# Kernel tuning notes

Measured on AMD Instinct MI355X. Metric: run time of the kernel, lower is better.

Reference implementation:

```python
import jax, jax.numpy as jnp
import numpy as np

BS = 8192
NUM_CLASSES = 400
D = 768


def _bilin_from_14(m14, Y, X, eH, eW):
    # Value of bilinear-resize(m14 -> (eH,eW)) at integer pixel (Y,X), computed on the fly.
    # torch F.interpolate(align_corners=False): src = (dst+0.5)*in/out - 0.5, clamped at 0.
    # m14: (bs,14,14); Y,X: (bs,14) float integer-valued coords; eH,eW: (bs,) float.
    sy = jnp.maximum((Y + 0.5) * 14.0 / eH[:, None] - 0.5, 0.0)
    sx = jnp.maximum((X + 0.5) * 14.0 / eW[:, None] - 0.5, 0.0)
    r0f = jnp.floor(sy); c0f = jnp.floor(sx)
    r0 = r0f.astype(jnp.int32); r1 = jnp.minimum(r0 + 1, 13)
    c0 = c0f.astype(jnp.int32); c1 = jnp.minimum(c0 + 1, 13)
    fy = sy - r0f; fx = sx - c0f
    b = jnp.arange(m14.shape[0])[:, None, None]
    g00 = m14[b, r0[:, :, None], c0[:, None, :]]
    g01 = m14[b, r0[:, :, None], c1[:, None, :]]
    g10 = m14[b, r1[:, :, None], c0[:, None, :]]
    g11 = m14[b, r1[:, :, None], c1[:, None, :]]
    wy = fy[:, :, None]; wx = fx[:, None, :]
    return g00 * (1 - wy) * (1 - wx) + g01 * (1 - wy) * wx + g10 * wy * (1 - wx) + g11 * wy * wx


def _get_mask(attn, o_pos, e_pos):
    # Fused, fully-batched equivalent of the per-sample python loop:
    #   resize 14x14 -> (eH,eW) bilinear; crop (top,left,oH,oW); resize -> 14x14 bilinear.
    # The final resize only reads the intermediate grid at 4 integer points per output
    # pixel, so we evaluate those points lazily via _bilin_from_14 (exact, no Emax grid).
    bs = attn.shape[0]
    m14 = attn.reshape(bs, 14, 14)
    eH = e_pos[:, 2].astype(jnp.float32); eW = e_pos[:, 3].astype(jnp.float32)
    top = (o_pos[:, 0] - e_pos[:, 0]).astype(jnp.float32)
    left = (o_pos[:, 1] - e_pos[:, 1]).astype(jnp.float32)
    oH = o_pos[:, 2].astype(jnp.float32); oW = o_pos[:, 3].astype(jnp.float32)
    i = jnp.arange(14, dtype=jnp.float32)[None, :]
    ty = jnp.maximum((i + 0.5) * oH[:, None] / 14.0 - 0.5, 0.0)  # (bs,14) coords in crop
    tx = jnp.maximum((i + 0.5) * oW[:, None] / 14.0 - 0.5, 0.0)
    y0 = jnp.floor(ty); y1 = jnp.minimum(y0 + 1.0, oH[:, None] - 1.0); wy = ty - y0
    x0 = jnp.floor(tx); x1 = jnp.minimum(x0 + 1.0, oW[:, None] - 1.0); wx = tx - x0
    Y0 = top[:, None] + y0; Y1 = top[:, None] + y1  # absolute rows in (eH,eW) grid
    X0 = left[:, None] + x0; X1 = left[:, None] + x1
    v00 = _bilin_from_14(m14, Y0, X0, eH, eW)
    v01 = _bilin_from_14(m14, Y0, X1, eH, eW)
    v10 = _bilin_from_14(m14, Y1, X0, eH, eW)
    v11 = _bilin_from_14(m14, Y1, X1, eH, eW)
    wyc = wy[:, :, None]; wxc = wx[:, None, :]
    out = v00 * (1 - wyc) * (1 - wxc) + v01 * (1 - wyc) * wxc + v10 * wyc * (1 - wxc) + v11 * wyc * wxc
    return out.reshape(bs, 196)


def _get_att_mask(attention, ratio=0.5):
    bs = attention.shape[0]
    a14 = attention.reshape(bs, 14, 14)
    # bilinear 14->7 with align_corners=False samples at frac 0.5 == 2x2 average pool
    a7 = a14.reshape(bs, 7, 2, 7, 2).mean(axis=(2, 4))
    flat = a7.reshape(bs, 49)
    n_keep = int(49 * ratio) + 1  # argsort desc, take top N+1 = 25
    _, idx = jax.lax.top_k(flat, n_keep)
    masks = jnp.ones((bs, 49), dtype=bool)
    masks = masks.at[jnp.arange(bs)[:, None], idx].set(False)
    m7 = masks.reshape(bs, 7, 7)
    full = jnp.repeat(jnp.repeat(m7, 2, axis=1), 2, axis=2)
    return full.reshape(bs, 196)


def setup_inputs() -> dict:
    key = jax.random.key(0)
    k1, k2, k3 = jax.random.split(key, 3)
    attn = jax.random.uniform(k1, (BS, 196), dtype=jnp.float32)
    rng = np.random.default_rng(0)
    IMG = 224
    eH = rng.integers(112, IMG + 1, BS); eW = rng.integers(112, IMG + 1, BS)
    eT = rng.integers(0, IMG - eH + 1); eL = rng.integers(0, IMG - eW + 1)
    def box():
        h = rng.integers(56, eH + 1); w = rng.integers(56, eW + 1)
        t = eT + rng.integers(0, eH - h + 1); l = eL + rng.integers(0, eW - w + 1)
        return np.stack([t, l, h, w], axis=1)
    e = np.stack([eT, eL, eH, eW], axis=1)
    pos = np.stack([box(), box(), e], axis=1).astype(np.int32)  # (BS,3,4)
    image_embed = jax.random.normal(k2, (2 * BS, D), dtype=jnp.float32)
    W = jax.random.normal(k3, (NUM_CLASSES, D), dtype=jnp.float32) * 0.02
    b = jnp.zeros((NUM_CLASSES,), dtype=jnp.float32)
    return {"attn": attn, "pos": jnp.asarray(pos), "image_embed": image_embed, "W": W, "b": b}


def reference(attn, pos, image_embed, W, b):
    cm1 = _get_mask(attn, pos[:, 0], pos[:, 2])
    mask1 = _get_att_mask(cm1)
    cm2 = _get_mask(attn, pos[:, 1], pos[:, 2])
    mask2 = _get_att_mask(cm2)
    mask = jnp.concatenate([mask1, mask2], axis=0)  # (2*bs,196) bool, fed to masked encoder
    logits = image_embed @ W.T + b
    return logits, mask
```

## Files before the change

kernel.cpp:

```cpp
#include <hip/hip_runtime.h>
#include <hip/hip_bf16.h>
#include <stdint.h>
#include <type_traits>

#define BSAMP 8192
#define NCLS 400
#define DIM 768
#define LOGITS_SIZE (16384LL * 400LL)
#define GEMM_BLOCKS 1280
#define MASK_BLOCKS 4096
#define W_ELEMS (NCLS * DIM)

typedef __attribute__((ext_vector_type(8))) short short8;
typedef __attribute__((ext_vector_type(4))) float floatx4;

__device__ inline unsigned int packbf(float a, float b) {
    unsigned int ua = __float_as_uint(a) + 0x8000u;
    unsigned int ub = __float_as_uint(b) + 0x8000u;
    return __builtin_amdgcn_perm(ub, ua, 0x07060302u);
}

__device__ inline short8 cvt8(float4 lo, float4 hi) {
    union { unsigned int u[4]; short8 s; } r;
    r.u[0] = packbf(lo.x, lo.y);
    r.u[1] = packbf(lo.z, lo.w);
    r.u[2] = packbf(hi.x, hi.y);
    r.u[3] = packbf(hi.z, hi.w);
    return r.s;
}

__device__ inline void gload16(const void* g, void* l) {
    __builtin_amdgcn_global_load_lds((const __attribute__((address_space(1))) void*)g,
                                     (__attribute__((address_space(3))) void*)l, 16, 0, 0);
}

__global__ void cvtW_kernel(const float* __restrict__ W, unsigned short* __restrict__ ws) {
    int i = (blockIdx.x * 256 + threadIdx.x) * 4;
    if (i < W_ELEMS) {
        float4 f = *(const float4*)(W + i);
        uint2 r;
        r.x = packbf(f.x, f.y);
        r.y = packbf(f.z, f.w);
        *(uint2*)(ws + i) = r;
    }
}

__device__ inline float tap4(const float* m14, int r0, int c0, float fy, float fx) {
    int r1 = min(r0 + 1, 13);
    int c1 = min(c0 + 1, 13);
    float g00 = m14[r0 * 14 + c0];
    float g01 = m14[r0 * 14 + c1];
    float g10 = m14[r1 * 14 + c0];
    float g11 = m14[r1 * 14 + c1];
    return g00 * (1.f - fy) * (1.f - fx) + g01 * (1.f - fy) * fx +
           g10 * fy * (1.f - fx) + g11 * fy * fx;
}

struct GemmSm { unsigned short B[2][4][80 * 32]; };

template <bool USE_WS>
__global__ __launch_bounds__(256, 4) void gemm_kernel(const float* __restrict__ E,
                                                      const float* __restrict__ W,
                                                      const float* __restrict__ bias,
                                                      const unsigned short* __restrict__ wsW,
                                                      float* __restrict__ out) {
    __shared__ __align__(16) GemmSm sg;

    const int bx = blockIdx.x;
    const int t  = threadIdx.x;
    const int wv = t >> 6, ln = t & 63;

    const int xcd = bx & 7;
    const int j   = bx >> 3;
    const int n0  = (j % 5) * 80;
    const int m0  = (xcd * 32 + j / 5) * 64;
    const int quad = ln >> 4, l16 = ln & 15;

    const float* aptr = E + (size_t)(m0 + wv * 16 + l16) * DIM + quad * 8;

    floatx4 acc[5];
#pragma unroll
    for (int ni = 0; ni < 5; ++ni) acc[ni] = (floatx4){0.f, 0.f, 0.f, 0.f};

    if constexpr (USE_WS) {
        auto stageB = [&](int s, int buf) {
            unsigned short* dst = &sg.B[buf][wv][0];
            const int rr = ln >> 2, ch = ln & 3;
#pragma unroll
            for (int c = 0; c < 5; ++c) {
                int row = c * 16 + rr;
                const unsigned short* src = wsW + (size_t)(n0 + row) * DIM +
                                            s * 128 + wv * 32 + 8 * (ch ^ ((row >> 1) & 3));
                gload16(src, dst + c * 512);
            }
        };

        float4 pf[2][2];
        auto LDA = [&](int it, int d) {
            pf[d][0] = *(const float4*)(aptr + it * 32);
            pf[d][1] = *(const float4*)(aptr + it * 32 + 4);
        };

        stageB(0, 0);
        LDA(0, 0);
        LDA(1, 1);
        __syncthreads();

#pragma unroll
        for (int s = 0; s < 6; ++s) {
            if (s < 5) stageB(s + 1, (s + 1) & 1);
#pragma unroll
            for (int j4 = 0; j4 < 4; ++j4) {
                const int it = s * 4 + j4;
                const int pb = it & 1;
                short8 af = cvt8(pf[pb][0], pf[pb][1]);
                if (it < 22) LDA(it + 2, pb);
                __builtin_amdgcn_sched_barrier(0);
                const unsigned short* bb = &sg.B[s & 1][j4][0];
#pragma unroll
                for (int ni = 0; ni < 5; ++ni) {
                    int row = ni * 16 + l16;
                    short8 bfr = *(const short8*)(bb + row * 32 + 8 * (quad ^ ((row >> 1) & 3)));
                    acc[ni] = __builtin_amdgcn_mfma_f32_16x16x32_bf16(af, bfr, acc[ni], 0, 0, 0);
                }
            }
            __syncthreads();
        }
    } else {
#pragma unroll 4
        for (int it = 0; it < 24; ++it) {
            short8 af = cvt8(*(const float4*)(aptr + it * 32), *(const float4*)(aptr + it * 32 + 4));
#pragma unroll
            for (int ni = 0; ni < 5; ++ni) {
                const float* wp = W + (size_t)(n0 + ni * 16 + l16) * DIM + it * 32 + quad * 8;
                short8 bfr = cvt8(*(const float4*)wp, *(const float4*)(wp + 4));
                acc[ni] = __builtin_amdgcn_mfma_f32_16x16x32_bf16(af, bfr, acc[ni], 0, 0, 0);
            }
        }
    }

    const int rowBase = m0 + wv * 16 + quad * 4;
#pragma unroll
    for (int ni = 0; ni < 5; ++ni) {
        int col = n0 + ni * 16 + l16;
        float bv = bias[col];
#pragma unroll
        for (int r = 0; r < 4; ++r) {
            out[(size_t)(rowBase + r) * NCLS + col] = acc[ni][r] + bv;
        }
    }
}

struct MaskSm { float m14[4][208]; float a7[4][56]; float mv[4][56]; };

__global__ __launch_bounds__(256, 8) void mask_kernel(const float* __restrict__ attn,
                                                      const int* __restrict__ pos,
                                                      float* __restrict__ out) {
    __shared__ __align__(16) MaskSm sm;

    const int bx = blockIdx.x;
    const int t  = threadIdx.x;
    const int wv = t >> 6, ln = t & 63;

    const int p = bx * 4 + wv;
    const int b = p >> 1;
    const int o = p & 1;
    float* m14 = sm.m14[wv];

    for (int i = ln; i < 196; i += 64) m14[i] = attn[(size_t)b * 196 + i];

    const int* pb = pos + (size_t)b * 12;
    const float topf  = (float)(pb[o * 4 + 0] - pb[8]);
    const float leftf = (float)(pb[o * 4 + 1] - pb[9]);
    const float oH = (float)pb[o * 4 + 2];
    const float oW = (float)pb[o * 4 + 3];
    const float eH = (float)pb[10];
    const float eW = (float)pb[11];
    __syncthreads();

    const int i7 = ln / 7, j7 = ln - i7 * 7;
    if (ln < 49) {
        int   cI[2][2];  float cF[2][2];  float wxs[2];
        int   rI[2][2];  float rF[2][2];  float wys[2];
#pragma unroll
        for (int dx = 0; dx < 2; ++dx) {
            int ox = 2 * j7 + dx;
            float tx = fmaxf((ox + 0.5f) * oW / 14.0f - 0.5f, 0.0f);
            float x0 = floorf(tx);
            float x1 = fminf(x0 + 1.0f, oW - 1.0f);
            wxs[dx] = tx - x0;
            float X0 = leftf + x0, X1 = leftf + x1;
            float sx0 = fmaxf((X0 + 0.5f) * 14.0f / eW - 0.5f, 0.0f);
            float c0f = floorf(sx0);
            cI[dx][0] = (int)c0f; cF[dx][0] = sx0 - c0f;
            float sx1 = fmaxf((X1 + 0.5f) * 14.0f / eW - 0.5f, 0.0f);
            float c1f = floorf(sx1);
            cI[dx][1] = (int)c1f; cF[dx][1] = sx1 - c1f;
        }
#pragma unroll
        for (int dy = 0; dy < 2; ++dy) {
            int oy = 2 * i7 + dy;
            float ty = fmaxf((oy + 0.5f) * oH / 14.0f - 0.5f, 0.0f);
            float y0 = floorf(ty);
            float y1 = fminf(y0 + 1.0f, oH - 1.0f);
            wys[dy] = ty - y0;
            float Y0 = topf + y0, Y1 = topf + y1;
            float sy0 = fmaxf((Y0 + 0.5f) * 14.0f / eH - 0.5f, 0.0f);
            float r0f = floorf(sy0);
            rI[dy][0] = (int)r0f; rF[dy][0] = sy0 - r0f;
            float sy1 = fmaxf((Y1 + 0.5f) * 14.0f / eH - 0.5f, 0.0f);
            float r1f = floorf(sy1);
            rI[dy][1] = (int)r1f; rF[dy][1] = sy1 - r1f;
        }

        float s = 0.f;
#pragma unroll
        for (int dy = 0; dy < 2; ++dy) {
            float wy = wys[dy];
#pragma unroll
            for (int dx = 0; dx < 2; ++dx) {
                float wx = wxs[dx];
                float v00 = tap4(m14, rI[dy][0], cI[dx][0], rF[dy][0], cF[dx][0]);
                float v01 = tap4(m14, rI[dy][0], cI[dx][1], rF[dy][0], cF[dx][1]);
                float v10 = tap4(m14, rI[dy][1], cI[dx][0], rF[dy][1], cF[dx][0]);
                float v11 = tap4(m14, rI[dy][1], cI[dx][1], rF[dy][1], cF[dx][1]);
                float cm = v00 * (1.f - wy) * (1.f - wx) + v01 * (1.f - wy) * wx +
                           v10 * wy * (1.f - wx) + v11 * wy * wx;
                s += cm;
            }
        }
        sm.a7[wv][ln] = s * 0.25f;
    }
    __syncthreads();

    if (ln < 49) {
        float mine = sm.a7[wv][ln];
        int cnt = 0;
#pragma unroll 7
        for (int s2 = 0; s2 < 49; ++s2) {
            float v = sm.a7[wv][s2];
            cnt += (v > mine) || (v == mine && s2 < ln);
        }
        sm.mv[wv][ln] = (cnt < 25) ? 0.0f : 1.0f;
    }
    __syncthreads();

    float* ob = out + LOGITS_SIZE + (size_t)(o * BSAMP + b) * 196;
    for (int i = ln; i < 196; i += 64) {
        int oy = i / 14, ox = i - oy * 14;
        ob[i] = sm.mv[wv][(oy >> 1) * 7 + (ox >> 1)];
    }
}

extern "C" void kernel_launch(void* const* d_in, const int* in_sizes, int n_in,
                              void* d_out, int out_size, void* d_ws, size_t ws_size,
                              hipStream_t stream) {
    const float* attn = (const float*)d_in[0];
    const int*   pos  = (const int*)d_in[1];
    const float* E    = (const float*)d_in[2];
    const float* W    = (const float*)d_in[3];
    const float* bias = (const float*)d_in[4];
    float* out = (float*)d_out;

    if (ws_size >= (size_t)W_ELEMS * 2) {
        unsigned short* ws = (unsigned short*)d_ws;
        cvtW_kernel<<<300, 256, 0, stream>>>(W, ws);
        gemm_kernel<true><<<GEMM_BLOCKS, 256, 0, stream>>>(E, W, bias, ws, out);
    } else {
        gemm_kernel<false><<<GEMM_BLOCKS, 256, 0, stream>>>(E, W, bias, nullptr, out);
    }
    mask_kernel<<<MASK_BLOCKS, 256, 0, stream>>>(attn, pos, out);
}
```

Measured before the change: 165.8 us.

## Compute full 400-column output per block so activations are read once

After: 147.3 us. 1.13x faster.

```diff
diff --git a/kernel.cpp b/kernel.cpp
--- a/kernel.cpp
+++ b/kernel.cpp
@@ -7,7 +7,7 @@
 #define NCLS 400
 #define DIM 768
 #define LOGITS_SIZE (16384LL * 400LL)
-#define GEMM_BLOCKS 1280
+#define GEMM_BLOCKS 256
 #define MASK_BLOCKS 4096
 #define W_ELEMS (NCLS * DIM)
 
@@ -56,10 +56,10 @@
            g10 * fy * (1.f - fx) + g11 * fy * fx;
 }
 
-struct GemmSm { unsigned short B[2][4][80 * 32]; };
+struct GemmSm { unsigned short B[2][400 * 64]; };
 
 template <bool USE_WS>
-__global__ __launch_bounds__(256, 4) void gemm_kernel(const float* __restrict__ E,
+__global__ __launch_bounds__(256, 1) void gemm_kernel(const float* __restrict__ E,
                                                       const float* __restrict__ W,
                                                       const float* __restrict__ bias,
                                                       const unsigned short* __restrict__ wsW,
@@ -70,28 +70,24 @@
     const int t  = threadIdx.x;
     const int wv = t >> 6, ln = t & 63;
 
-    const int xcd = bx & 7;
-    const int j   = bx >> 3;
-    const int n0  = (j % 5) * 80;
-    const int m0  = (xcd * 32 + j / 5) * 64;
+    const int m0 = bx * 64;
     const int quad = ln >> 4, l16 = ln & 15;
 
     const float* aptr = E + (size_t)(m0 + wv * 16 + l16) * DIM + quad * 8;
 
-    floatx4 acc[5];
-#pragma unroll
-    for (int ni = 0; ni < 5; ++ni) acc[ni] = (floatx4){0.f, 0.f, 0.f, 0.f};
+    floatx4 acc[25];
+#pragma unroll
+    for (int ni = 0; ni < 25; ++ni) acc[ni] = (floatx4){0.f, 0.f, 0.f, 0.f};
 
     if constexpr (USE_WS) {
         auto stageB = [&](int s, int buf) {
-            unsigned short* dst = &sg.B[buf][wv][0];
-            const int rr = ln >> 2, ch = ln & 3;
-#pragma unroll
-            for (int c = 0; c < 5; ++c) {
-                int row = c * 16 + rr;
-                const unsigned short* src = wsW + (size_t)(n0 + row) * DIM +
-                                            s * 128 + wv * 32 + 8 * (ch ^ ((row >> 1) & 3));
-                gload16(src, dst + c * 512);
+            unsigned short* base = &sg.B[buf][0];
+            for (int c = wv; c < 50; c += 4) {
+                int row = c * 8 + (ln >> 3);
+                const unsigned short* src = wsW + (size_t)row * DIM + s * 64 +
+                                            ((ln >> 2) & 1) * 32 +
+                                            8 * ((ln & 3) ^ ((row >> 1) & 3));
+                gload16(src, base + c * 512);
             }
         };
 
@@ -107,32 +103,32 @@
         __syncthreads();
 
 #pragma unroll
-        for (int s = 0; s < 6; ++s) {
-            if (s < 5) stageB(s + 1, (s + 1) & 1);
-#pragma unroll
-            for (int j4 = 0; j4 < 4; ++j4) {
-                const int it = s * 4 + j4;
+        for (int s = 0; s < 12; ++s) {
+            if (s < 11) stageB(s + 1, (s + 1) & 1);
+#pragma unroll
+            for (int kk = 0; kk < 2; ++kk) {
+                const int it = s * 2 + kk;
                 const int pb = it & 1;
                 short8 af = cvt8(pf[pb][0], pf[pb][1]);
                 if (it < 22) LDA(it + 2, pb);
                 __builtin_amdgcn_sched_barrier(0);
-                const unsigned short* bb = &sg.B[s & 1][j4][0];
-#pragma unroll
-                for (int ni = 0; ni < 5; ++ni) {
+                const unsigned short* bb = &sg.B[s & 1][0];
+#pragma unroll
+                for (int ni = 0; ni < 25; ++ni) {
                     int row = ni * 16 + l16;
-                    short8 bfr = *(const short8*)(bb + row * 32 + 8 * (quad ^ ((row >> 1) & 3)));
+                    short8 bfr = *(const short8*)(bb + row * 64 + kk * 32 +
+                                                  8 * (quad ^ ((row >> 1) & 3)));
                     acc[ni] = __builtin_amdgcn_mfma_f32_16x16x32_bf16(af, bfr, acc[ni], 0, 0, 0);
                 }
             }
             __syncthreads();
         }
     } else {
-#pragma unroll 4
         for (int it = 0; it < 24; ++it) {
             short8 af = cvt8(*(const float4*)(aptr + it * 32), *(const float4*)(aptr + it * 32 + 4));
 #pragma unroll
-            for (int ni = 0; ni < 5; ++ni) {
-                const float* wp = W + (size_t)(n0 + ni * 16 + l16) * DIM + it * 32 + quad * 8;
+            for (int ni = 0; ni < 25; ++ni) {
+                const float* wp = W + (size_t)(ni * 16 + l16) * DIM + it * 32 + quad * 8;
                 short8 bfr = cvt8(*(const float4*)wp, *(const float4*)(wp + 4));
                 acc[ni] = __builtin_amdgcn_mfma_f32_16x16x32_bf16(af, bfr, acc[ni], 0, 0, 0);
             }
@@ -141,8 +137,8 @@
 
     const int rowBase = m0 + wv * 16 + quad * 4;
 #pragma unroll
-    for (int ni = 0; ni < 5; ++ni) {
-        int col = n0 + ni * 16 + l16;
+    for (int ni = 0; ni < 25; ++ni) {
+        int col = ni * 16 + l16;
         float bv = bias[col];
 #pragma unroll
         for (int r = 0; r < 4; ++r) {
```
